# Kernel tuning notes

Hardware: AMD Instinct MI355X
Metric: run time of the kernel (lower is better)

Reference implementation:

```python
import jax, jax.numpy as jnp
import numpy as np

EPS = 1e-8
NUM_HEADS = 8
BELIEF_DIM = 256
TOP_K = 64
DEPTH_BIAS = 0.1


def setup_inputs() -> dict:
    key = jax.random.key(0)
    ks = jax.random.split(key, 12)
    B, T, H = 4, 2048, 2048
    N, D, h = 4096, BELIEF_DIM, NUM_HEADS
    G = 16
    s = 0.02
    return {
        'hidden': jax.random.normal(ks[0], (B, T, H), jnp.float32),
        'active_beliefs': jax.random.normal(ks[1], (N, D), jnp.float32),
        'goal_embeddings': jax.random.normal(ks[2], (G, D), jnp.float32),
        'goal_priorities': jax.random.uniform(ks[3], (G,), jnp.float32),
        'Wq': jax.random.normal(ks[4], (D * h, H), jnp.float32) * s,
        'Wo': jax.random.normal(ks[5], (H, D * h), jnp.float32) * s,
        'Wgoal': jax.random.normal(ks[6], (h, D), jnp.float32) * s,
        'log_temp': jnp.zeros((h,), jnp.float32),
        'Wu': jax.random.normal(ks[7], (H, D * h), jnp.float32) * s,
        'Wg1': jax.random.normal(ks[8], (H // 4, H), jnp.float32) * s,
        'bg1': jnp.zeros((H // 4,), jnp.float32),
        'Wg2': jax.random.normal(ks[9], (1, H // 4), jnp.float32) * s,
        'bg2': jnp.full((1,), 2.0, jnp.float32),  # read_gate_init_bias
        'conv_w': jax.random.normal(ks[10], (D * h, 1, 4), jnp.float32) * s,
    }


def reference(hidden, active_beliefs, goal_embeddings, goal_priorities,
              Wq, Wo, Wgoal, log_temp, Wu, Wg1, bg1, Wg2, bg2, conv_w):
    B, T, H = hidden.shape
    h, D = NUM_HEADS, BELIEF_DIM
    C = h * D

    # hyperspherical decomposition of active beliefs
    radii = jnp.maximum(jnp.linalg.norm(active_beliefs, axis=-1), EPS)  # [N]
    angles = active_beliefs / radii[:, None]                            # [N, D]

    # rough top-k selection (N_active > top_k path)
    mean_q = hidden.mean(axis=(0, 1)) @ Wq.T                 # [h*D]
    rough_q = mean_q.reshape(h, D).mean(axis=0)              # [D]
    rough_scores = angles @ rough_q                          # [N]
    _, topk = jax.lax.top_k(rough_scores, TOP_K)
    keys = angles[topk]              # [K, D]
    values = active_beliefs[topk]    # [K, D]

    # read gate: Linear -> ReLU -> Linear, then signed-sqrt + sigmoid
    g = jax.nn.relu(hidden @ Wg1.T + bg1) @ Wg2.T + bg2      # [B, T, 1]
    g = jnp.sign(g) * jnp.sqrt(jnp.maximum(jnp.abs(g), 1e-6))
    gate = jax.nn.sigmoid(g)

    # per-head queries and temperature-scaled Hopfield scores
    queries = (hidden @ Wq.T).reshape(B, T, h, D)
    temp = jnp.maximum(jnp.exp(log_temp + DEPTH_BIAS), 0.1)  # [h]
    scores = jnp.einsum('bthd,nd->bthn', queries, keys) / jnp.sqrt(jnp.float32(D))
    scores = scores * temp[None, None, :, None]

    # goal-directed bias
    goal_radii = jnp.maximum(jnp.linalg.norm(goal_embeddings, axis=-1), EPS)
    goal_angles = goal_embeddings / goal_radii[:, None]      # [G, D]
    sim = (keys @ goal_angles.T) * goal_priorities[None, :]  # [K, G]
    max_goal_sim = sim.max(axis=-1)                          # [K]
    gate_w = jax.nn.sigmoid(Wgoal @ goal_angles.mean(axis=0))  # [h]
    goal_bias = gate_w[:, None] * max_goal_sim[None, :]      # [h, K]
    scores = scores + goal_bias[None, None, :, :]

    attn = jax.nn.softmax(scores, axis=-1)                   # [B, T, h, K]
    retrieved = jnp.einsum('bthn,nd->bthd', attn, values)    # [B, T, h, D]
    flat = retrieved.reshape(B, T, C)

    # depthwise causal conv (kernel=4, left pad 3) + SiLU fusion
    x = jnp.transpose(flat, (0, 2, 1))                       # [B, C, T]
    conv = jax.lax.conv_general_dilated(
        x, conv_w, window_strides=(1,), padding=[(3, 0)],
        feature_group_count=C, dimension_numbers=('NCH', 'OIH', 'NCH'))
    flat = flat + jax.nn.silu(jnp.transpose(conv, (0, 2, 1)))

    output = gate * (flat @ Wo.T)                            # [B, T, H]
    utility_logits = flat @ Wu.T                             # [B, T, H]
    return output, utility_logits, attn, retrieved
```

## Files before the change

kernel.cpp:

```cpp
#include <hip/hip_runtime.h>


typedef unsigned short ushort_t;
typedef unsigned int   uint_t;

typedef __bf16 bf16x8 __attribute__((ext_vector_type(8)));
typedef float  f32x4  __attribute__((ext_vector_type(4)));
typedef unsigned short u16x8 __attribute__((ext_vector_type(8)));
typedef unsigned short u16x4 __attribute__((ext_vector_type(4)));

#define DI static __device__ __forceinline__

DI ushort_t f2bf(float f) {
    union { float f; uint_t u; } v; v.f = f;
    uint_t u = v.u;
    uint_t r = (u + 0x7FFFu + ((u >> 16) & 1u)) >> 16;
    return (ushort_t)r;
}
DI float bf2f(ushort_t b) {
    union { uint_t u; float f; } v; v.u = ((uint_t)b) << 16;
    return v.f;
}

#define GLL16(gp, lp) __builtin_amdgcn_global_load_lds( \
    (const __attribute__((address_space(1))) void*)(gp), \
    (__attribute__((address_space(3))) void*)(lp), 16, 0, 0)

constexpr int BT  = 8192;
constexpr int Hd  = 2048;
constexpr int Dd  = 256;
constexpr int Cd  = 2048;

constexpr size_t O_HID     = 0;
constexpr size_t O_WQ      = 33554432;
constexpr size_t O_WOWU    = 41943040;
constexpr size_t O_WG1     = 58720256;
constexpr size_t O_QRY     = 60817408;
constexpr size_t O_MEANACC = 94371840;
constexpr size_t O_MEANQ   = 94380032;
constexpr size_t O_RAD     = 94389248;
constexpr size_t O_RSC     = 94405632;
constexpr size_t O_KEYS    = 94422016;
constexpr size_t O_VALT    = 94454784;
constexpr size_t O_GB      = 94487552;
constexpr size_t O_HS      = 94489600;
constexpr size_t O_GP      = 94489856;

__global__ void cast4_kernel(const float* __restrict__ sA, ushort_t* __restrict__ dA, int nA,
                             const float* __restrict__ sB, ushort_t* __restrict__ dB, int nB,
                             const float* __restrict__ sC, ushort_t* __restrict__ dC, int nC,
                             const float* __restrict__ sD, ushort_t* __restrict__ dD, int nD) {
    int total = (nA + nB + nC + nD) >> 2;
    for (int i = blockIdx.x * blockDim.x + threadIdx.x; i < total;
         i += gridDim.x * blockDim.x) {
        int e = i * 4;
        const float* s; ushort_t* d;
        if (e < nA)              { s = sA + e; d = dA + e; }
        else if ((e -= nA) < nB) { s = sB + e; d = dB + e; }
        else if ((e -= nB) < nC) { s = sC + e; d = dC + e; }
        else                     { e -= nC; s = sD + e; d = dD + e; }
        float4 v = *(const float4*)s;
        u16x4 o;
        o[0] = f2bf(v.x); o[1] = f2bf(v.y); o[2] = f2bf(v.z); o[3] = f2bf(v.w);
        *(u16x4*)d = o;
    }
}

__global__ void cast_hidden_kernel(const float* __restrict__ hid, ushort_t* __restrict__ hbf,
                                   float* __restrict__ macc) {
    int r0 = blockIdx.x * 16;
    float s[8];
#pragma unroll
    for (int j = 0; j < 8; ++j) s[j] = 0.f;
    for (int r = 0; r < 16; ++r) {
        const float* rp = hid + (size_t)(r0 + r) * Hd;
        ushort_t*    wp = hbf + (size_t)(r0 + r) * Hd;
#pragma unroll
        for (int j = 0; j < 2; ++j) {
            int c = j * 1024 + threadIdx.x * 4;
            float4 v = *(const float4*)(rp + c);
            s[j*4+0] += v.x; s[j*4+1] += v.y; s[j*4+2] += v.z; s[j*4+3] += v.w;
            u16x4 o;
            o[0] = f2bf(v.x); o[1] = f2bf(v.y); o[2] = f2bf(v.z); o[3] = f2bf(v.w);
            *(u16x4*)(wp + c) = o;
        }
    }
#pragma unroll
    for (int j = 0; j < 2; ++j)
#pragma unroll
        for (int q = 0; q < 4; ++q)
            atomicAdd(macc + j * 1024 + threadIdx.x * 4 + q, s[j*4+q]);
}

__global__ void meanq_kernel(const float* __restrict__ macc, const float* __restrict__ Wq,
                             float* __restrict__ mq) {
    int wid = blockIdx.x * 4 + (threadIdx.x >> 6);
    int lane = threadIdx.x & 63;
    const float inv = 1.f / 8192.f;
    float s = 0.f;
    for (int k = lane; k < Hd; k += 64) s += macc[k] * inv * Wq[(size_t)wid * Hd + k];
#pragma unroll
    for (int m = 32; m; m >>= 1) s += __shfl_xor(s, m, 64);
    if (lane == 0) mq[wid] = s;
}

__global__ void beliefs_kernel(const float* __restrict__ ab, const float* __restrict__ mq,
                               float* __restrict__ radii, float* __restrict__ rsc) {
    int n = blockIdx.x * 4 + (threadIdx.x >> 6);
    int lane = threadIdx.x & 63;
    float rqv[4];
#pragma unroll
    for (int j = 0; j < 4; ++j) {
        int d = lane + 64 * j;
        float s = 0.f;
#pragma unroll
        for (int hh = 0; hh < 8; ++hh) s += mq[hh * 256 + d];
        rqv[j] = s * 0.125f;
    }
    float v[4]; float r2 = 0.f;
#pragma unroll
    for (int j = 0; j < 4; ++j) { v[j] = ab[(size_t)n * Dd + lane + 64 * j]; r2 += v[j] * v[j]; }
#pragma unroll
    for (int m = 32; m; m >>= 1) r2 += __shfl_xor(r2, m, 64);
    float r = fmaxf(sqrtf(r2), 1e-8f);
    float dq = 0.f;
#pragma unroll
    for (int j = 0; j < 4; ++j) dq += (v[j] / r) * rqv[j];
#pragma unroll
    for (int m = 32; m; m >>= 1) dq += __shfl_xor(dq, m, 64);
    if (lane == 0) { radii[n] = r; rsc[n] = dq; }
}

__global__ void topk_kernel(const float* __restrict__ ab, const float* __restrict__ radii,
                            const float* __restrict__ rsc, const float* __restrict__ gemb,
                            const float* __restrict__ gprio, const float* __restrict__ Wgoal,
                            const float* __restrict__ ltemp,
                            ushort_t* __restrict__ keysg, ushort_t* __restrict__ valtg,
                            float* __restrict__ gbias, float* __restrict__ hscale) {
    __shared__ float s_sc[4096];
    __shared__ float s_rv[4];
    __shared__ int   s_ri[4];
    __shared__ int   s_top[64];
    __shared__ float s_ga[16 * 256];
    __shared__ float s_mga[256];
    __shared__ float s_gw[8];
    __shared__ float s_keyf[64 * 256];
    __shared__ float s_red[256];

    int t = threadIdx.x;
    int lane = t & 63, w = t >> 6;
    for (int it = 0; it < 16; ++it) s_sc[t + it * 256] = rsc[t + it * 256];
    __syncthreads();

    for (int kk = 0; kk < 64; ++kk) {
        float bv = -3.4e38f; int bi = 0x7fffffff;
#pragma unroll
        for (int j4 = 0; j4 < 4; ++j4) {
            f32x4 v4 = *(const f32x4*)&s_sc[t * 16 + j4 * 4];
#pragma unroll
            for (int q = 0; q < 4; ++q) {
                int idx = t * 16 + j4 * 4 + q;
                float v = v4[q];
                if (v > bv || (v == bv && idx < bi)) { bv = v; bi = idx; }
            }
        }
#pragma unroll
        for (int m = 32; m; m >>= 1) {
            float ov = __shfl_xor(bv, m, 64);
            int   oi = __shfl_xor(bi, m, 64);
            if (ov > bv || (ov == bv && oi < bi)) { bv = ov; bi = oi; }
        }
        if (lane == 0) { s_rv[w] = bv; s_ri[w] = bi; }
        __syncthreads();
        if (t == 0) {
            float fv = s_rv[0]; int fi = s_ri[0];
#pragma unroll
            for (int wv = 1; wv < 4; ++wv)
                if (s_rv[wv] > fv || (s_rv[wv] == fv && s_ri[wv] < fi)) { fv = s_rv[wv]; fi = s_ri[wv]; }
            s_top[kk] = fi; s_sc[fi] = -3.4e38f;
        }
        __syncthreads();
    }

    {
        int kk = t >> 2, dp = t & 3;
        int idx = s_top[kk];
        float r = radii[idx];
        const float4* src = (const float4*)(ab + (size_t)idx * Dd + dp * 64);
#pragma unroll 4
        for (int dd = 0; dd < 16; ++dd) {
            float4 v = src[dd];
            int d = dp * 64 + dd * 4;
            float k0 = v.x / r, k1 = v.y / r, k2 = v.z / r, k3 = v.w / r;
            s_keyf[kk * 256 + d + 0] = k0;
            s_keyf[kk * 256 + d + 1] = k1;
            s_keyf[kk * 256 + d + 2] = k2;
            s_keyf[kk * 256 + d + 3] = k3;
            u16x4 o;
            o[0] = f2bf(k0); o[1] = f2bf(k1); o[2] = f2bf(k2); o[3] = f2bf(k3);
            *(u16x4*)(keysg + kk * 256 + d) = o;
            valtg[(d + 0) * 64 + kk] = f2bf(v.x);
            valtg[(d + 1) * 64 + kk] = f2bf(v.y);
            valtg[(d + 2) * 64 + kk] = f2bf(v.z);
            valtg[(d + 3) * 64 + kk] = f2bf(v.w);
        }
    }
    {
        for (int g = w; g < 16; g += 4) {
            float v[4]; float r2 = 0.f;
#pragma unroll
            for (int j = 0; j < 4; ++j) { v[j] = gemb[g * 256 + lane + 64 * j]; r2 += v[j] * v[j]; }
#pragma unroll
            for (int m = 32; m; m >>= 1) r2 += __shfl_xor(r2, m, 64);
            float r = fmaxf(sqrtf(r2), 1e-8f);
#pragma unroll
            for (int j = 0; j < 4; ++j) s_ga[g * 256 + lane + 64 * j] = v[j] / r;
        }
    }
    __syncthreads();
    {
        float s = 0.f;
        for (int g = 0; g < 16; ++g) s += s_ga[g * 256 + t];
        s_mga[t] = s * (1.f / 16.f);
    }
    __syncthreads();
    if (t < 8) {
        float s = 0.f;
        for (int d = 0; d < 256; ++d) s += Wgoal[t * 256 + d] * s_mga[d];
        s_gw[t] = 1.f / (1.f + expf(-s));
        hscale[t] = fmaxf(expf(ltemp[t] + 0.1f), 0.1f) * (1.f / 16.f);
    }
    __syncthreads();
    {
        int kk = t & 63, gq = t >> 6;
        const f32x4* kp = (const f32x4*)&s_keyf[kk * 256];
        float best = -3.4e38f;
        for (int g = gq * 4; g < gq * 4 + 4; ++g) {
            const f32x4* gp_ = (const f32x4*)&s_ga[g * 256];
            float dot = 0.f;
            for (int d4 = 0; d4 < 64; ++d4) {
                f32x4 a = kp[d4], b = gp_[d4];
                dot += a[0] * b[0] + a[1] * b[1] + a[2] * b[2] + a[3] * b[3];
            }
            best = fmaxf(best, dot * gprio[g]);
        }
        s_red[t] = best;
    }
    __syncthreads();
    if (t < 64) {
        float m = fmaxf(fmaxf(s_red[t], s_red[t + 64]), fmaxf(s_red[t + 128], s_red[t + 192]));
        for (int hh = 0; hh < 8; ++hh) gbias[hh * 64 + t] = s_gw[hh] * m;
    }
}

template <int EPI>
__global__ __launch_bounds__(256)
void gemm_bt_kernel(const ushort_t* __restrict__ A, const ushort_t* __restrict__ Bw,
                    const ushort_t* __restrict__ Bw2, int Kd,
                    ushort_t* __restrict__ obf, float* __restrict__ of1, float* __restrict__ of2,
                    const float* __restrict__ bg1, const float* __restrict__ Wg2,
                    float* __restrict__ gpart, const float* __restrict__ bg2) {
    __shared__ ushort_t lA[128 * 32];
    __shared__ ushort_t lB[128 * 32];
    const int tid = threadIdx.x;
    const int lane = tid & 63;
    const int w = tid >> 6;
    const int wr = (w >> 1) * 64, wc = (w & 1) * 64;

    const int nwg = gridDim.x * gridDim.y;
    const int lin = blockIdx.y * gridDim.x + blockIdx.x;
    const int swz = (lin & 7) * (nwg >> 3) + (lin >> 3);
    const int bm = (swz / gridDim.x) * 128, bn = (swz % gridDim.x) * 128;

    f32x4 acc[4][4];
#pragma unroll
    for (int mi = 0; mi < 4; ++mi)
#pragma unroll
        for (int ni = 0; ni < 4; ++ni)
#pragma unroll
            for (int q = 0; q < 4; ++q) acc[mi][ni][q] = 0.f;

    const ushort_t* Ab = A + (size_t)bm * Kd;
    const ushort_t* Bb;
    if (EPI == 3 && bn >= 2048) Bb = Bw2 + (size_t)(bn - 2048) * Kd;
    else                        Bb = Bw + (size_t)bn * Kd;
    const int c0 = tid, c1 = tid + 256;

    for (int kt = 0; kt < Kd; kt += 32) {
        __syncthreads();
        GLL16(Ab + (size_t)(c0 >> 2) * Kd + kt + (c0 & 3) * 8, lA + c0 * 8);
        GLL16(Ab + (size_t)(c1 >> 2) * Kd + kt + (c1 & 3) * 8, lA + c1 * 8);
        GLL16(Bb + (size_t)(c0 >> 2) * Kd + kt + (c0 & 3) * 8, lB + c0 * 8);
        GLL16(Bb + (size_t)(c1 >> 2) * Kd + kt + (c1 & 3) * 8, lB + c1 * 8);
        __syncthreads();
        const int ko = (lane >> 4) * 8;
        bf16x8 af[4], bf[4];
#pragma unroll
        for (int mi = 0; mi < 4; ++mi)
            af[mi] = *(const bf16x8*)&lA[(wr + mi * 16 + (lane & 15)) * 32 + ko];
#pragma unroll
        for (int ni = 0; ni < 4; ++ni)
            bf[ni] = *(const bf16x8*)&lB[(wc + ni * 16 + (lane & 15)) * 32 + ko];
#pragma unroll
        for (int mi = 0; mi < 4; ++mi)
#pragma unroll
            for (int ni = 0; ni < 4; ++ni)
                acc[mi][ni] = __builtin_amdgcn_mfma_f32_16x16x32_bf16(af[mi], bf[ni], acc[mi][ni], 0, 0, 0);
    }

    if (EPI == 2) {
        const float b2 = bg2[0];
#pragma unroll
        for (int mi = 0; mi < 4; ++mi)
#pragma unroll
            for (int r = 0; r < 4; ++r) {
                int row = bm + wr + mi * 16 + (lane >> 4) * 4 + r;
                float g = gpart[row] + b2;
                float sg = (g > 0.f) ? 1.f : ((g < 0.f) ? -1.f : 0.f);
                float ss = sg * sqrtf(fmaxf(fabsf(g), 1e-6f));
                float gv = 1.f / (1.f + expf(-ss));
#pragma unroll
                for (int ni = 0; ni < 4; ++ni) {
                    int col = bn + wc + ni * 16 + (lane & 15);
                    float v = acc[mi][ni][r];
                    if (col < 2048) of1[(size_t)row * 2048 + col] = gv * v;
                    else            of2[(size_t)row * 2048 + (col - 2048)] = v;
                }
            }
    } else {
        if (bn < 2048) {
#pragma unroll
            for (int mi = 0; mi < 4; ++mi)
#pragma unroll
                for (int ni = 0; ni < 4; ++ni)
#pragma unroll
                    for (int r = 0; r < 4; ++r) {
                        int row = bm + wr + mi * 16 + (lane >> 4) * 4 + r;
                        int col = bn + wc + ni * 16 + (lane & 15);
                        obf[(size_t)row * 2048 + col] = f2bf(acc[mi][ni][r]);
                    }
        } else {
            float wg[4], bb[4];
#pragma unroll
            for (int ni = 0; ni < 4; ++ni) {
                int col = bn + wc + ni * 16 + (lane & 15) - 2048;
                wg[ni] = Wg2[col]; bb[ni] = bg1[col];
            }
#pragma unroll
            for (int mi = 0; mi < 4; ++mi)
#pragma unroll
                for (int r = 0; r < 4; ++r) {
                    float s = 0.f;
#pragma unroll
                    for (int ni = 0; ni < 4; ++ni) {
                        float v = acc[mi][ni][r] + bb[ni];
                        v = fmaxf(v, 0.f);
                        s += v * wg[ni];
                    }
#pragma unroll
                    for (int m = 8; m; m >>= 1) s += __shfl_xor(s, m, 64);
                    if ((lane & 15) == 0)
                        atomicAdd(gpart + bm + wr + mi * 16 + (lane >> 4) * 4 + r, s);
                }
        }
    }
}

__global__ __launch_bounds__(256, 2)
void attn_kernel(const ushort_t* __restrict__ qry, const ushort_t* __restrict__ keysg,
                 const ushort_t* __restrict__ valtg, const float* __restrict__ gbias,
                 const float* __restrict__ hscale, float* __restrict__ attn_out,
                 float* __restrict__ retr_out, ushort_t* __restrict__ flatb) {
    __shared__ ushort_t sK[64 * 256];
    __shared__ ushort_t sV[256 * 64];
    __shared__ ushort_t sP[4][32 * 64];

    const int tid = threadIdx.x, lane = tid & 63, w = tid >> 6;
    const int r0 = blockIdx.x * 32;
    const int head = blockIdx.y * 4 + w;

    for (int it = 0; it < 8; ++it) {
        int f = it * 256 + tid;
        int row = f >> 5, cb = f & 31;
        u16x8 v = *(const u16x8*)(keysg + f * 8);
        int byte = (row * 512 + cb * 16) ^ ((row & 7) << 4);
        *(u16x8*)((char*)sK + byte) = v;
    }
    for (int it = 0; it < 8; ++it) {
        int f = it * 256 + tid;
        int row = f >> 3, cb = f & 7;
        u16x8 v = *(const u16x8*)(valtg + f * 8);
        int byte = (row * 128 + cb * 16) ^ ((row & 7) << 4);
        *(u16x8*)((char*)sV + byte) = v;
    }
    __syncthreads();

    char* sPw = (char*)sP[w];
    const float hs = hscale[head];
    float gb[4];
#pragma unroll
    for (int ni = 0; ni < 4; ++ni) gb[ni] = gbias[head * 64 + ni * 16 + (lane & 15)];

    const ushort_t* qbase = qry + (size_t)r0 * Cd + head * 256
                          + (size_t)(lane & 15) * Cd + (lane >> 4) * 8;

    f32x4 accs[2][4];
#pragma unroll
    for (int mi = 0; mi < 2; ++mi)
#pragma unroll
        for (int ni = 0; ni < 4; ++ni)
#pragma unroll
            for (int q = 0; q < 4; ++q) accs[mi][ni][q] = 0.f;

#pragma unroll
    for (int kt = 0; kt < 8; ++kt) {
        const int kb = kt * 64 + (lane >> 4) * 16;
        bf16x8 aq[2], bk[4];
#pragma unroll
        for (int mi = 0; mi < 2; ++mi)
            aq[mi] = *(const bf16x8*)(qbase + (size_t)(mi * 16) * Cd + kt * 32);
#pragma unroll
        for (int ni = 0; ni < 4; ++ni) {
            int n = ni * 16 + (lane & 15);
            bk[ni] = *(const bf16x8*)((const char*)sK + ((n * 512 + kb) ^ ((n & 7) << 4)));
        }
#pragma unroll
        for (int mi = 0; mi < 2; ++mi)
#pragma unroll
            for (int ni = 0; ni < 4; ++ni)
                accs[mi][ni] = __builtin_amdgcn_mfma_f32_16x16x32_bf16(aq[mi], bk[ni], accs[mi][ni], 0, 0, 0);
    }

#pragma unroll
    for (int mi = 0; mi < 2; ++mi)
#pragma unroll
        for (int r = 0; r < 4; ++r) {
            float sc[4];
            float mx = -3.4e38f;
#pragma unroll
            for (int ni = 0; ni < 4; ++ni) {
                sc[ni] = accs[mi][ni][r] * hs + gb[ni];
                mx = fmaxf(mx, sc[ni]);
            }
#pragma unroll
            for (int m = 8; m; m >>= 1) mx = fmaxf(mx, __shfl_xor(mx, m, 64));
            float p[4]; float sm = 0.f;
#pragma unroll
            for (int ni = 0; ni < 4; ++ni) { p[ni] = expf(sc[ni] - mx); sm += p[ni]; }
#pragma unroll
            for (int m = 8; m; m >>= 1) sm += __shfl_xor(sm, m, 64);
            float inv = 1.f / sm;
            int row = mi * 16 + (lane >> 4) * 4 + r;
            size_t ob = (size_t)(r0 + row) * 512 + head * 64;
#pragma unroll
            for (int ni = 0; ni < 4; ++ni) {
                float a = p[ni] * inv;
                int col = ni * 16 + (lane & 15);
                attn_out[ob + col] = a;
                int byte = (row * 128 + col * 2) ^ ((row & 7) << 4);
                *(ushort_t*)(sPw + byte) = f2bf(a);
            }
        }

    f32x4 accr[2][16];
#pragma unroll
    for (int mi = 0; mi < 2; ++mi)
#pragma unroll
        for (int ni = 0; ni < 16; ++ni)
#pragma unroll
            for (int q = 0; q < 4; ++q) accr[mi][ni][q] = 0.f;

#pragma unroll
    for (int kt = 0; kt < 2; ++kt) {
        const int kb = kt * 64 + (lane >> 4) * 16;
        bf16x8 ap[2];
#pragma unroll
        for (int mi = 0; mi < 2; ++mi) {
            int m = mi * 16 + (lane & 15);
            ap[mi] = *(const bf16x8*)(sPw + ((m * 128 + kb) ^ ((m & 7) << 4)));
        }
#pragma unroll
        for (int ni = 0; ni < 16; ++ni) {
            int n = ni * 16 + (lane & 15);
            bf16x8 bv = *(const bf16x8*)((const char*)sV + ((n * 128 + kb) ^ ((n & 7) << 4)));
            accr[0][ni] = __builtin_amdgcn_mfma_f32_16x16x32_bf16(ap[0], bv, accr[0][ni], 0, 0, 0);
            accr[1][ni] = __builtin_amdgcn_mfma_f32_16x16x32_bf16(ap[1], bv, accr[1][ni], 0, 0, 0);
        }
    }

#pragma unroll
    for (int mi = 0; mi < 2; ++mi)
#pragma unroll
        for (int ni = 0; ni < 16; ++ni)
#pragma unroll
            for (int r = 0; r < 4; ++r) {
                int row = mi * 16 + (lane >> 4) * 4 + r;
                int d = ni * 16 + (lane & 15);
                float v = accr[mi][ni][r];
                size_t o = (size_t)(r0 + row) * Cd + head * 256 + d;
                retr_out[o] = v;
                flatb[o] = f2bf(v);
            }
}

__global__ void conv_kernel(const ushort_t* __restrict__ flat, const float* __restrict__ cw,
                            ushort_t* __restrict__ flat2) {
    int cq = blockIdx.x * 256 + threadIdx.x;
    int c  = cq * 4;
    int b  = blockIdx.z;
    int t0 = blockIdx.y * 32;
    float4 wv[4];
#pragma unroll
    for (int j = 0; j < 4; ++j) wv[j] = *(const float4*)(cw + (size_t)(c + j) * 4);
    size_t base = (size_t)b * 2048 * Cd + c;
    float xm3[4], xm2[4], xm1[4];
    if (t0 == 0) {
#pragma unroll
        for (int j = 0; j < 4; ++j) { xm3[j] = 0.f; xm2[j] = 0.f; xm1[j] = 0.f; }
    } else {
        u16x4 a3 = *(const u16x4*)(flat + base + (size_t)(t0 - 3) * Cd);
        u16x4 a2 = *(const u16x4*)(flat + base + (size_t)(t0 - 2) * Cd);
        u16x4 a1 = *(const u16x4*)(flat + base + (size_t)(t0 - 1) * Cd);
#pragma unroll
        for (int j = 0; j < 4; ++j) { xm3[j] = bf2f(a3[j]); xm2[j] = bf2f(a2[j]); xm1[j] = bf2f(a1[j]); }
    }
    for (int t = t0; t < t0 + 32; ++t) {
        u16x4 xv = *(const u16x4*)(flat + base + (size_t)t * Cd);
        u16x4 ov;
#pragma unroll
        for (int j = 0; j < 4; ++j) {
            float x = bf2f(xv[j]);
            float cv = wv[j].x * xm3[j] + wv[j].y * xm2[j] + wv[j].z * xm1[j] + wv[j].w * x;
            float sl = cv / (1.f + expf(-cv));
            ov[j] = f2bf(x + sl);
            xm3[j] = xm2[j]; xm2[j] = xm1[j]; xm1[j] = x;
        }
        *(u16x4*)(flat2 + base + (size_t)t * Cd) = ov;
    }
}

extern "C" void kernel_launch(void* const* d_in, const int* in_sizes, int n_in,
                              void* d_out, int out_size, void* d_ws, size_t ws_size,
                              hipStream_t stream) {
    (void)in_sizes; (void)n_in; (void)out_size; (void)ws_size;
    const float* hid   = (const float*)d_in[0];
    const float* ab    = (const float*)d_in[1];
    const float* gemb  = (const float*)d_in[2];
    const float* gprio = (const float*)d_in[3];
    const float* Wq    = (const float*)d_in[4];
    const float* Wo    = (const float*)d_in[5];
    const float* Wgoal = (const float*)d_in[6];
    const float* ltemp = (const float*)d_in[7];
    const float* Wu    = (const float*)d_in[8];
    const float* Wg1   = (const float*)d_in[9];
    const float* bg1   = (const float*)d_in[10];
    const float* Wg2   = (const float*)d_in[11];
    const float* bg2   = (const float*)d_in[12];
    const float* cw    = (const float*)d_in[13];

    float* out      = (float*)d_out;
    float* out_util = out + 16777216;
    float* out_attn = out + 33554432;
    float* out_retr = out + 37748736;

    char* ws = (char*)d_ws;
    ushort_t* hbf    = (ushort_t*)(ws + O_HID);
    ushort_t* wqb    = (ushort_t*)(ws + O_WQ);
    ushort_t* wowub  = (ushort_t*)(ws + O_WOWU);
    ushort_t* wg1b   = (ushort_t*)(ws + O_WG1);
    ushort_t* qryb   = (ushort_t*)(ws + O_QRY);
    ushort_t* flatb  = hbf;
    float* macc   = (float*)(ws + O_MEANACC);
    float* meanq  = (float*)(ws + O_MEANQ);
    float* radii  = (float*)(ws + O_RAD);
    float* rsc    = (float*)(ws + O_RSC);
    ushort_t* keysb = (ushort_t*)(ws + O_KEYS);
    ushort_t* valtb = (ushort_t*)(ws + O_VALT);
    float* gbias  = (float*)(ws + O_GB);
    float* hscale = (float*)(ws + O_HS);
    float* gpart  = (float*)(ws + O_GP);

    hipMemsetAsync(ws + O_MEANACC, 0, 2048 * 4, stream);
    hipMemsetAsync(ws + O_GP, 0, 8192 * 4, stream);

    cast_hidden_kernel<<<512, 256, 0, stream>>>(hid, hbf, macc);
    cast4_kernel<<<2048, 256, 0, stream>>>(Wq, wqb, 2048 * 2048,
                                           Wo, wowub, 2048 * 2048,
                                           Wu, wowub + 2048 * 2048, 2048 * 2048,
                                           Wg1, wg1b, 512 * 2048);

    meanq_kernel<<<512, 256, 0, stream>>>(macc, Wq, meanq);
    beliefs_kernel<<<1024, 256, 0, stream>>>(ab, meanq, radii, rsc);
    topk_kernel<<<1, 256, 0, stream>>>(ab, radii, rsc, gemb, gprio, Wgoal, ltemp,
                                       keysb, valtb, gbias, hscale);

    gemm_bt_kernel<3><<<dim3(20, 64), 256, 0, stream>>>(hbf, wqb, wg1b, 2048,
        qryb, nullptr, nullptr, bg1, Wg2, gpart, nullptr);

    attn_kernel<<<dim3(256, 2), 256, 0, stream>>>(qryb, keysb, valtb, gbias, hscale,
                                                  out_attn, out_retr, flatb);

    conv_kernel<<<dim3(2, 64, 4), 256, 0, stream>>>(flatb, cw, qryb );

    gemm_bt_kernel<2><<<dim3(32, 64), 256, 0, stream>>>(qryb, wowub, nullptr, 2048,
        nullptr, out, out_util, nullptr, nullptr, gpart, bg2);
}
```

Before: 904.3 us.

## Rewrite GEMM with 256x256 tiles, triple-buffered LDS prefetch and swizzled layout

The bf16 GEMM kernel moves from 128x128 tiles with 256 threads and a single LDS buffer to 256x256 tiles with 512 threads. It adds a three-slot LDS ring that prefetches two K-steps ahead via async global-to-LDS loads, an XOR swizzle on LDS columns to reduce bank conflicts, and s_setprio around the MFMA block. The two workspace memsets are merged into one larger memset. The larger tiles raise per-thread register use (32 accumulators) and LDS footprint, and the 10x32 grid for the first GEMM leaves fewer workgroups to fill the CUs.

```diff
diff --git a/kernel.cpp b/kernel.cpp
--- a/kernel.cpp
+++ b/kernel.cpp
@@ -45,6 +45,7 @@
 constexpr size_t O_GB      = 94487552;
 constexpr size_t O_HS      = 94489600;
 constexpr size_t O_GP      = 94489856;
+constexpr size_t MEMSET_SZ = 94522624 - O_MEANACC;
 
 __global__ void cast4_kernel(const float* __restrict__ sA, ushort_t* __restrict__ dA, int nA,
                              const float* __restrict__ sB, ushort_t* __restrict__ dB, int nB,
@@ -254,64 +255,101 @@
 }
 
 template <int EPI>
-__global__ __launch_bounds__(256)
+__global__ __launch_bounds__(512, 2)
 void gemm_bt_kernel(const ushort_t* __restrict__ A, const ushort_t* __restrict__ Bw,
                     const ushort_t* __restrict__ Bw2, int Kd,
                     ushort_t* __restrict__ obf, float* __restrict__ of1, float* __restrict__ of2,
                     const float* __restrict__ bg1, const float* __restrict__ Wg2,
                     float* __restrict__ gpart, const float* __restrict__ bg2) {
-    __shared__ ushort_t lA[128 * 32];
-    __shared__ ushort_t lB[128 * 32];
-    const int tid = threadIdx.x;
+    __shared__ __align__(16) ushort_t lds[3 * 16384];
+
+    const int tid  = threadIdx.x;
     const int lane = tid & 63;
-    const int w = tid >> 6;
-    const int wr = (w >> 1) * 64, wc = (w & 1) * 64;
+    const int w    = tid >> 6;
+    const int wr   = (w >> 2) * 128;
+    const int wc   = (w & 3) * 64;
 
     const int nwg = gridDim.x * gridDim.y;
     const int lin = blockIdx.y * gridDim.x + blockIdx.x;
     const int swz = (lin & 7) * (nwg >> 3) + (lin >> 3);
-    const int bm = (swz / gridDim.x) * 128, bn = (swz % gridDim.x) * 128;
-
-    f32x4 acc[4][4];
-#pragma unroll
-    for (int mi = 0; mi < 4; ++mi)
-#pragma unroll
-        for (int ni = 0; ni < 4; ++ni)
-#pragma unroll
-            for (int q = 0; q < 4; ++q) acc[mi][ni][q] = 0.f;
+    const int bm = (swz / gridDim.x) * 256, bn = (swz % gridDim.x) * 256;
 
     const ushort_t* Ab = A + (size_t)bm * Kd;
     const ushort_t* Bb;
     if (EPI == 3 && bn >= 2048) Bb = Bw2 + (size_t)(bn - 2048) * Kd;
     else                        Bb = Bw + (size_t)bn * Kd;
-    const int c0 = tid, c1 = tid + 256;
-
-    for (int kt = 0; kt < Kd; kt += 32) {
-        __syncthreads();
-        GLL16(Ab + (size_t)(c0 >> 2) * Kd + kt + (c0 & 3) * 8, lA + c0 * 8);
-        GLL16(Ab + (size_t)(c1 >> 2) * Kd + kt + (c1 & 3) * 8, lA + c1 * 8);
-        GLL16(Bb + (size_t)(c0 >> 2) * Kd + kt + (c0 & 3) * 8, lB + c0 * 8);
-        GLL16(Bb + (size_t)(c1 >> 2) * Kd + kt + (c1 & 3) * 8, lB + c1 * 8);
-        __syncthreads();
-        const int ko = (lane >> 4) * 8;
-        bf16x8 af[4], bf[4];
-#pragma unroll
-        for (int mi = 0; mi < 4; ++mi)
-            af[mi] = *(const bf16x8*)&lA[(wr + mi * 16 + (lane & 15)) * 32 + ko];
+
+    const int c0 = tid, c1 = tid + 512;
+    const int r0s = c0 >> 2, r1s = c1 >> 2;
+    const int cbl0 = (c0 & 3) ^ (r0s & 3) ^ ((r0s >> 2) & 3);
+    const int cbl1 = (c1 & 3) ^ (r1s & 3) ^ ((r1s >> 2) & 3);
+    const size_t src0 = (size_t)r0s * Kd + cbl0 * 8;
+    const size_t src1 = (size_t)r1s * Kd + cbl1 * 8;
+
+    const int pcb = (lane >> 4) ^ (lane & 3) ^ ((lane >> 2) & 3);
+    const int aBase = (wr + (lane & 15)) * 32 + pcb * 8;
+    const int bBase = 8192 + (wc + (lane & 15)) * 32 + pcb * 8;
+
+    f32x4 acc[8][4];
+#pragma unroll
+    for (int mi = 0; mi < 8; ++mi)
 #pragma unroll
         for (int ni = 0; ni < 4; ++ni)
-            bf[ni] = *(const bf16x8*)&lB[(wc + ni * 16 + (lane & 15)) * 32 + ko];
-#pragma unroll
-        for (int mi = 0; mi < 4; ++mi)
+#pragma unroll
+            for (int q = 0; q < 4; ++q) acc[mi][ni][q] = 0.f;
+
+    const int NT = Kd >> 5;
+
+#define STAGE_T(t_, slot_) do {                                            \
+        const ushort_t* As_ = Ab + (size_t)(t_) * 32;                      \
+        const ushort_t* Bs_ = Bb + (size_t)(t_) * 32;                      \
+        ushort_t* ls_ = lds + (slot_) * 16384;                             \
+        GLL16(As_ + src0, ls_ + c0 * 8);                                   \
+        GLL16(As_ + src1, ls_ + c1 * 8);                                   \
+        GLL16(Bs_ + src0, ls_ + 8192 + c0 * 8);                            \
+        GLL16(Bs_ + src1, ls_ + 8192 + c1 * 8);                            \
+    } while (0)
+
+    STAGE_T(0, 0);
+    STAGE_T(1, 1);
+
+    int slot = 0;
+    for (int t = 0; t < NT; ++t) {
+        if (t >= NT - 2) asm volatile("s_waitcnt vmcnt(0)" ::: "memory");
+        else             asm volatile("s_waitcnt vmcnt(4)" ::: "memory");
+        __builtin_amdgcn_s_barrier();
+        __builtin_amdgcn_sched_barrier(0);
+
+        const ushort_t* sl = lds + slot * 16384;
+        bf16x8 afr[8], bfr[4];
+#pragma unroll
+        for (int mi = 0; mi < 8; ++mi)
+            afr[mi] = *(const bf16x8*)(sl + aBase + mi * 512);
+#pragma unroll
+        for (int ni = 0; ni < 4; ++ni)
+            bfr[ni] = *(const bf16x8*)(sl + bBase + ni * 512);
+
+        if (t + 2 < NT) {
+            int s2 = slot + 2; if (s2 >= 3) s2 -= 3;
+            STAGE_T(t + 2, s2);
+        }
+
+        __builtin_amdgcn_s_setprio(1);
+#pragma unroll
+        for (int mi = 0; mi < 8; ++mi)
 #pragma unroll
             for (int ni = 0; ni < 4; ++ni)
-                acc[mi][ni] = __builtin_amdgcn_mfma_f32_16x16x32_bf16(af[mi], bf[ni], acc[mi][ni], 0, 0, 0);
-    }
+                acc[mi][ni] = __builtin_amdgcn_mfma_f32_16x16x32_bf16(afr[mi], bfr[ni], acc[mi][ni], 0, 0, 0);
+        __builtin_amdgcn_s_setprio(0);
+
+        ++slot; if (slot >= 3) slot = 0;
+    }
+#undef STAGE_T
 
     if (EPI == 2) {
         const float b2 = bg2[0];
 #pragma unroll
-        for (int mi = 0; mi < 4; ++mi)
+        for (int mi = 0; mi < 8; ++mi)
 #pragma unroll
             for (int r = 0; r < 4; ++r) {
                 int row = bm + wr + mi * 16 + (lane >> 4) * 4 + r;
@@ -330,7 +368,7 @@
     } else {
         if (bn < 2048) {
 #pragma unroll
-            for (int mi = 0; mi < 4; ++mi)
+            for (int mi = 0; mi < 8; ++mi)
 #pragma unroll
                 for (int ni = 0; ni < 4; ++ni)
 #pragma unroll
@@ -347,7 +385,7 @@
                 wg[ni] = Wg2[col]; bb[ni] = bg1[col];
             }
 #pragma unroll
-            for (int mi = 0; mi < 4; ++mi)
+            for (int mi = 0; mi < 8; ++mi)
 #pragma unroll
                 for (int r = 0; r < 4; ++r) {
                     float s = 0.f;
@@ -580,8 +618,7 @@
     float* hscale = (float*)(ws + O_HS);
     float* gpart  = (float*)(ws + O_GP);
 
-    hipMemsetAsync(ws + O_MEANACC, 0, 2048 * 4, stream);
-    hipMemsetAsync(ws + O_GP, 0, 8192 * 4, stream);
+    hipMemsetAsync(ws + O_MEANACC, 0, MEMSET_SZ, stream);
 
     cast_hidden_kernel<<<512, 256, 0, stream>>>(hid, hbf, macc);
     cast4_kernel<<<2048, 256, 0, stream>>>(Wq, wqb, 2048 * 2048,
@@ -594,7 +631,7 @@
     topk_kernel<<<1, 256, 0, stream>>>(ab, radii, rsc, gemb, gprio, Wgoal, ltemp,
                                        keysb, valtb, gbias, hscale);
 
-    gemm_bt_kernel<3><<<dim3(20, 64), 256, 0, stream>>>(hbf, wqb, wg1b, 2048,
+    gemm_bt_kernel<3><<<dim3(10, 32), 512, 0, stream>>>(hbf, wqb, wg1b, 2048,
         qryb, nullptr, nullptr, bg1, Wg2, gpart, nullptr);
 
     attn_kernel<<<dim3(256, 2), 256, 0, stream>>>(qryb, keysb, valtb, gbias, hscale,
@@ -602,6 +639,6 @@
 
     conv_kernel<<<dim3(2, 64, 4), 256, 0, stream>>>(flatb, cw, qryb );
 
-    gemm_bt_kernel<2><<<dim3(32, 64), 256, 0, stream>>>(qryb, wowub, nullptr, 2048,
+    gemm_bt_kernel<2><<<dim3(16, 32), 512, 0, stream>>>(qryb, wowub, nullptr, 2048,
         nullptr, out, out_util, nullptr, nullptr, gpart, bg2);
 }
```

New measurement: 877.3 us. -3.0%, faster.
